# Kernel optimization log

Hardware: AMD Instinct MI355X
Metric: run time of the kernel (lower is better)

## Reference

```python
import jax, jax.numpy as jnp
import numpy as np

N = 2000  # nodes per graph (hardcoded in the original module)


def gatv2(x, src, dst, edge_attr, Wl, Wr, We, att, b):
    """PyG GATv2Conv (concat=True, negative_slope=0.2, edge_dim) forward.
    x: [N, Fin]; src/dst: [E]; edge_attr: [E, 2]; att: [H, C]. Returns [N, H*C]."""
    n = x.shape[0]
    H, C = att.shape
    xl = (x @ Wl).reshape(n, H, C)            # messages from source nodes
    xr = (x @ Wr).reshape(n, H, C)            # target-node term
    ee = (edge_attr @ We).reshape(-1, H, C)   # edge feature term
    m = jax.nn.leaky_relu(xl[src] + xr[dst] + ee, 0.2)
    logits = jnp.einsum('ehc,hc->eh', m, att)           # [E, H]
    lmax = jax.ops.segment_max(logits, dst, num_segments=n)
    p = jnp.exp(logits - lmax[dst])
    denom = jax.ops.segment_sum(p, dst, num_segments=n)
    alpha = p / (denom[dst] + 1e-16)                    # scatter-softmax over in-edges
    out = jax.ops.segment_sum(alpha[:, :, None] * xl[src], dst, num_segments=n)
    return out.reshape(n, H * C) + b


def setup_inputs() -> dict:
    key = jax.random.key(0)
    ks = jax.random.split(key, 32)
    B, T, F, E = 4, 10, 8, 16000
    s = 0.05
    d = {
        'x': jax.random.normal(ks[0], (B, T, N, F), jnp.float32),
        'edge_index': jax.random.randint(ks[1], (2, E), 0, N, jnp.int32),
        'edge_attr': jax.random.normal(ks[2], (E, 2), jnp.float32),
        'w_l0': s * jax.random.normal(ks[3], (8, 128)),
        'w_r0': s * jax.random.normal(ks[4], (8, 128)),
        'w_e0': s * jax.random.normal(ks[5], (2, 128)),
        'att0': s * jax.random.normal(ks[6], (4, 32)),
        'b0': s * jax.random.normal(ks[7], (128,)),
        'w_l1': s * jax.random.normal(ks[8], (128, 128)),
        'w_r1': s * jax.random.normal(ks[9], (128, 128)),
        'w_e1': s * jax.random.normal(ks[10], (2, 128)),
        'att1': s * jax.random.normal(ks[11], (4, 32)),
        'b1': s * jax.random.normal(ks[12], (128,)),
        'w_l2': s * jax.random.normal(ks[13], (128, 32)),
        'w_r2': s * jax.random.normal(ks[14], (128, 32)),
        'w_e2': s * jax.random.normal(ks[15], (2, 32)),
        'att2': s * jax.random.normal(ks[16], (4, 8)),
        'b2': s * jax.random.normal(ks[17], (32,)),
        'w_ih': s * jax.random.normal(ks[18], (1024, 64000)),
        'w_hh': s * jax.random.normal(ks[19], (1024, 256)),
        'b_ih': s * jax.random.normal(ks[20], (1024,)),
        'b_hh': s * jax.random.normal(ks[21], (1024,)),
        'fc1_w': s * jax.random.normal(ks[22], (256, 512)),
        'fc1_b': s * jax.random.normal(ks[23], (512,)),
        'fc2_w': s * jax.random.normal(ks[24], (512, 1)),
        'fc2_b': s * jax.random.normal(ks[25], (1,)),
    }
    return d


def reference(x, edge_index, edge_attr, w_l0, w_r0, w_e0, att0, b0,
              w_l1, w_r1, w_e1, att1, b1, w_l2, w_r2, w_e2, att2, b2,
              w_ih, w_hh, b_ih, b_hh, fc1_w, fc1_b, fc2_w, fc2_b):
    B, T = x.shape[0], x.shape[1]
    # PyG GATv2Conv add_self_loops=True with fill_value='mean' for edge_attr
    loop = jnp.arange(N, dtype=edge_index.dtype)
    src = jnp.concatenate([edge_index[0], loop])
    dst = jnp.concatenate([edge_index[1], loop])
    ea = jnp.concatenate([edge_attr, jnp.broadcast_to(edge_attr.mean(0), (N, 2))], axis=0)

    def gat_stack(xt):  # [N, F] -> [N*32] flattened embedding
        h = jax.nn.relu(gatv2(xt, src, dst, ea, w_l0, w_r0, w_e0, att0, b0))
        h = jax.nn.relu(gatv2(h, src, dst, ea, w_l1, w_r1, w_e1, att1, b1))
        h = jax.nn.relu(gatv2(h, src, dst, ea, w_l2, w_r2, w_e2, att2, b2))
        return h.reshape(-1)

    emb = jax.vmap(jax.vmap(gat_stack))(x)  # [B, T, 64000]

    # single-layer LSTM (torch gate order: i, f, g, o)
    Hh = w_hh.shape[1]
    def step(carry, xt):
        h, c = carry
        g = xt @ w_ih.T + h @ w_hh.T + (b_ih + b_hh)
        i, f, gg, o = jnp.split(g, 4, axis=-1)
        c = jax.nn.sigmoid(f) * c + jax.nn.sigmoid(i) * jnp.tanh(gg)
        h = jax.nn.sigmoid(o) * jnp.tanh(c)
        return (h, c), h
    h0 = jnp.zeros((B, Hh), emb.dtype)
    (_, _), hs = jax.lax.scan(step, (h0, h0), jnp.swapaxes(emb, 0, 1))  # hs: [T, B, Hh]

    last = jax.nn.relu(hs[-1])                       # relu(lstm_out)[:, -1, :]
    hid = jax.nn.relu(last @ fc1_w + fc1_b)          # (dropout=0 -> identity)
    return hid @ fc2_w + fc2_b                       # [B, 1]
```

## Files before the change

kernel.cpp:

```cpp
#include <hip/hip_runtime.h>
#include <hip/hip_bf16.h>
#include <math.h>

typedef __hip_bfloat16 bf16;
typedef __attribute__((ext_vector_type(8))) short short8;
typedef __attribute__((ext_vector_type(4))) float f32x4;

#define NNODES 2000
#define NEDGE_IN 16000
#define NEDGE 18000
#define NGRAPH 40

__device__ __forceinline__ float bf2f(bf16 v){ return __bfloat162float(v); }
__device__ __forceinline__ bf16 f2bf(float v){ return __float2bfloat16(v); }
__device__ __forceinline__ short bfbits(float v){ bf16 t = __float2bfloat16(v); return *reinterpret_cast<short*>(&t); }

__global__ __launch_bounds__(256) void k_setup(const float* __restrict__ ea, float* __restrict__ mean_ea,
                        const float* __restrict__ whh, unsigned* __restrict__ whhT2,
                        const float* __restrict__ w1a, const float* __restrict__ w1b,
                        const float* __restrict__ w2a, const float* __restrict__ w2b,
                        bf16* __restrict__ b1a, bf16* __restrict__ b1b,
                        bf16* __restrict__ b2a, bf16* __restrict__ b2b,
                        int* __restrict__ cnt, int* __restrict__ cursor, float* __restrict__ gates){
  int bb = blockIdx.x, tid = threadIdx.x;
  if (bb == 0){
    __shared__ float s0l[256], s1l[256];
    float s0=0.f, s1=0.f;
    for (int e = tid; e < NEDGE_IN; e += 256){ s0 += ea[2*e]; s1 += ea[2*e+1]; }
    s0l[tid]=s0; s1l[tid]=s1; __syncthreads();
    for (int d=128; d>=1; d>>=1){
      if (tid < d){ s0l[tid]+=s0l[tid+d]; s1l[tid]+=s1l[tid+d]; }
      __syncthreads();
    }
    if (tid==0){ mean_ea[0]=s0l[0]/(float)NEDGE_IN; mean_ea[1]=s1l[0]/(float)NEDGE_IN; }
  } else if (bb < 513){
    int idx = (bb-1)*256 + tid;
    int j = idx >> 7, kp = idx & 127;
    unsigned ulo = (unsigned)(unsigned short)bfbits(whh[j*256 + 2*kp]);
    unsigned uhi = (unsigned)(unsigned short)bfbits(whh[j*256 + 2*kp + 1]);
    whhT2[kp*1024 + j] = (uhi<<16) | ulo;
  } else if (bb < 673){
    int idx = (bb-513)*256 + tid;
    const float* src; bf16* dst; int n, local;
    if (idx < 16384){ src=w1a; dst=b1a; n=128; local=idx; }
    else if (idx < 32768){ src=w1b; dst=b1b; n=128; local=idx-16384; }
    else if (idx < 36864){ src=w2a; dst=b2a; n=32; local=idx-32768; }
    else { src=w2b; dst=b2b; n=32; local=idx-36864; }
    int k = local / n, c = local % n;
    dst[c*128 + k] = f2bf(src[local]);
  } else {
    int idx = (bb-673)*256 + tid;
    if (idx < 2000) cnt[idx] = 0;
    else if (idx < 4000) cursor[idx-2000] = 0;
    else if (idx < 44960) gates[idx-4000] = 0.f;
  }
}

__global__ void k_count(const int* __restrict__ ei, int* __restrict__ cnt){
  int e = blockIdx.x*256 + threadIdx.x;
  if (e >= NEDGE) return;
  int d = (e < NEDGE_IN) ? ei[NEDGE_IN + e] : (e - NEDGE_IN);
  atomicAdd(&cnt[d], 1);
}

__global__ void k_scan(const int* __restrict__ cnt, int* __restrict__ off){
  __shared__ int s[2048];
  int lane = threadIdx.x;
  for (int i = lane; i < 2048; i += 64) s[i] = (i < NNODES) ? cnt[i] : 0;
  __syncthreads();
  int base = lane*32, run = 0;
  for (int j=0;j<32;j++){ int t = s[base+j]; s[base+j] = run; run += t; }
  int x = run;
  for (int d=1; d<64; d<<=1){ int y = __shfl_up(x, d); if (lane >= d) x += y; }
  int chunkOff = x - run;
  for (int j=0;j<32;j++){ int idx = base+j; if (idx <= NNODES) off[idx] = chunkOff + s[idx]; }
}

__global__ void k_scatter(const int* __restrict__ ei, const int* __restrict__ off,
                          int* __restrict__ cursor, const float* __restrict__ ea,
                          const float* __restrict__ mean_ea,
                          int* __restrict__ csr_src, float2* __restrict__ eaP){
  int e = blockIdx.x*256 + threadIdx.x;
  if (e >= NEDGE) return;
  int d, sn; float2 a;
  if (e < NEDGE_IN){ sn = ei[e]; d = ei[NEDGE_IN+e]; a = ((const float2*)ea)[e]; }
  else { sn = e-NEDGE_IN; d = sn; a.x = mean_ea[0]; a.y = mean_ea[1]; }
  int p = off[d] + atomicAdd(&cursor[d], 1);
  csr_src[p] = sn;
  eaP[p] = a;
}

__global__ __launch_bounds__(256) void k_gemm0(const float* __restrict__ X, const float* __restrict__ Wa,
                                               const float* __restrict__ Wb,
                                               bf16* __restrict__ Ya, bf16* __restrict__ Yb){
  __shared__ float Ws[2*8*128];
  for (int i = threadIdx.x; i < 8*128; i += 256){ Ws[i] = Wa[i]; Ws[1024+i] = Wb[i]; }
  __syncthreads();
  int j  = threadIdx.x % 128;
  int rg = threadIdx.x / 128;
  size_t m0 = (size_t)blockIdx.x*8 + (size_t)rg*4;
  const float* x0 = X + m0*8;
  float a0=0.f,a1=0.f,a2=0.f,a3=0.f, b0=0.f,b1=0.f,b2=0.f,b3=0.f;
  #pragma unroll
  for (int k=0;k<8;k++){
    float wa = Ws[k*128 + j], wb = Ws[1024 + k*128 + j];
    float x_0 = x0[k], x_1 = x0[8+k], x_2 = x0[16+k], x_3 = x0[24+k];
    a0 += x_0*wa; a1 += x_1*wa; a2 += x_2*wa; a3 += x_3*wa;
    b0 += x_0*wb; b1 += x_1*wb; b2 += x_2*wb; b3 += x_3*wb;
  }
  bf16* ya = Ya + m0*128 + j;
  bf16* yb = Yb + m0*128 + j;
  ya[0]=f2bf(a0); ya[128]=f2bf(a1); ya[256]=f2bf(a2); ya[384]=f2bf(a3);
  yb[0]=f2bf(b0); yb[128]=f2bf(b1); yb[256]=f2bf(b2); yb[384]=f2bf(b3);
}

template<int N>
__global__ __launch_bounds__(256) void k_gemm_mf2(const bf16* __restrict__ A, const bf16* __restrict__ BTa,
                                                  const bf16* __restrict__ BTb,
                                                  bf16* __restrict__ Ya, bf16* __restrict__ Yb){
  const int NT = N/16;
  int lane = threadIdx.x & 63, wv = threadIdx.x >> 6;
  size_t m0 = (size_t)blockIdx.x*128 + (size_t)wv*32;
  int r = lane & 15, kg = lane >> 4;
  const f32x4 zero = {0.f,0.f,0.f,0.f};
  f32x4 acca[2][NT], accb[2][NT];
  #pragma unroll
  for (int s=0;s<2;s++)
    #pragma unroll
    for (int t=0;t<NT;t++){ acca[s][t] = zero; accb[s][t] = zero; }
  #pragma unroll
  for (int c=0;c<4;c++){
    short8 a0 = *(const short8*)(A + (m0 + r)*128 + c*32 + kg*8);
    short8 a1 = *(const short8*)(A + (m0 + 16 + r)*128 + c*32 + kg*8);
    #pragma unroll
    for (int t=0;t<NT;t++){
      short8 ba = *(const short8*)(BTa + (size_t)(t*16 + r)*128 + c*32 + kg*8);
      short8 bb = *(const short8*)(BTb + (size_t)(t*16 + r)*128 + c*32 + kg*8);
      acca[0][t] = __builtin_amdgcn_mfma_f32_16x16x32_bf16(a0, ba, acca[0][t], 0,0,0);
      acca[1][t] = __builtin_amdgcn_mfma_f32_16x16x32_bf16(a1, ba, acca[1][t], 0,0,0);
      accb[0][t] = __builtin_amdgcn_mfma_f32_16x16x32_bf16(a0, bb, accb[0][t], 0,0,0);
      accb[1][t] = __builtin_amdgcn_mfma_f32_16x16x32_bf16(a1, bb, accb[1][t], 0,0,0);
    }
  }
  #pragma unroll
  for (int s=0;s<2;s++)
    #pragma unroll
    for (int t=0;t<NT;t++){
      size_t row = m0 + s*16 + kg*4;
      int col = t*16 + r;
      #pragma unroll
      for (int i=0;i<4;i++){
        Ya[(row+i)*N + col] = f2bf(acca[s][t][i]);
        Yb[(row+i)*N + col] = f2bf(accb[s][t][i]);
      }
    }
}

template<int H, int C>
__global__ __launch_bounds__(256) void k_edge(const bf16* __restrict__ XL, const bf16* __restrict__ XR,
                                              const float2* __restrict__ eaP, const int* __restrict__ off,
                                              const int* __restrict__ csr_src, const float* __restrict__ att,
                                              const float* __restrict__ We, const float* __restrict__ bias,
                                              bf16* __restrict__ Hout){
  const int HC = H*C;
  const int LPN = HC/2;
  const int NPW = 64/LPN;
  const int NPB = 4*NPW;
  int tid = threadIdx.x;
  int lane = tid & 63, wv = tid >> 6;
  int ln = lane % LPN;
  int n  = blockIdx.x*NPB + wv*NPW + lane/LPN;
  int g  = blockIdx.y;
  int c0 = 2*ln;
  size_t gbase = (size_t)g*NNODES*HC;
  const unsigned* XLu = (const unsigned*)(XL + gbase);
  unsigned xru = ((const unsigned*)(XR + gbase))[n*LPN + ln];
  float xr0 = __uint_as_float(xru<<16);
  float xr1 = __uint_as_float(xru & 0xffff0000u);
  float av0 = att[c0], av1 = att[c0+1];
  float w00 = We[c0], w01 = We[c0+1];
  float w10 = We[HC+c0], w11 = We[HC+c0+1];
  float srun = 0.f, acc0 = 0.f, acc1 = 0.f;
  int p0 = off[n], p1 = off[n+1];
  int p = p0;
  for (; p+2 <= p1; p += 2){
    int uA = csr_src[p], uB = csr_src[p+1];
    float2 eA = eaP[p], eB = eaP[p+1];
    unsigned xlA = XLu[uA*LPN + ln];
    unsigned xlB = XLu[uB*LPN + ln];
    float xa0 = __uint_as_float(xlA<<16), xa1 = __uint_as_float(xlA & 0xffff0000u);
    float xb0 = __uint_as_float(xlB<<16), xb1 = __uint_as_float(xlB & 0xffff0000u);
    float sa0 = xa0 + fmaf(eA.x,w00, fmaf(eA.y,w10, xr0));
    float sa1 = xa1 + fmaf(eA.x,w01, fmaf(eA.y,w11, xr1));
    float sb0 = xb0 + fmaf(eB.x,w00, fmaf(eB.y,w10, xr0));
    float sb1 = xb1 + fmaf(eB.x,w01, fmaf(eB.y,w11, xr1));
    float ma0 = sa0>0.f?sa0:0.2f*sa0, ma1 = sa1>0.f?sa1:0.2f*sa1;
    float mb0 = sb0>0.f?sb0:0.2f*sb0, mb1 = sb1>0.f?sb1:0.2f*sb1;
    float cA = fmaf(ma0,av0, ma1*av1);
    float cB = fmaf(mb0,av0, mb1*av1);
    #pragma unroll
    for (int d=C/4; d>=1; d>>=1){ cA += __shfl_xor(cA, d); cB += __shfl_xor(cB, d); }
    float peA = __expf(cA), peB = __expf(cB);
    srun += peA + peB;
    acc0 = fmaf(peA, xa0, fmaf(peB, xb0, acc0));
    acc1 = fmaf(peA, xa1, fmaf(peB, xb1, acc1));
  }
  if (p < p1){
    int uA = csr_src[p];
    float2 eA = eaP[p];
    unsigned xlA = XLu[uA*LPN + ln];
    float xa0 = __uint_as_float(xlA<<16), xa1 = __uint_as_float(xlA & 0xffff0000u);
    float sa0 = xa0 + fmaf(eA.x,w00, fmaf(eA.y,w10, xr0));
    float sa1 = xa1 + fmaf(eA.x,w01, fmaf(eA.y,w11, xr1));
    float ma0 = sa0>0.f?sa0:0.2f*sa0, ma1 = sa1>0.f?sa1:0.2f*sa1;
    float cA = fmaf(ma0,av0, ma1*av1);
    #pragma unroll
    for (int d=C/4; d>=1; d>>=1) cA += __shfl_xor(cA, d);
    float peA = __expf(cA);
    srun += peA;
    acc0 = fmaf(peA, xa0, acc0);
    acc1 = fmaf(peA, xa1, acc1);
  }
  float inv = 1.f/(srun + 1e-16f);
  float o0 = fmaf(acc0, inv, bias[c0]);
  float o1 = fmaf(acc1, inv, bias[c0+1]);
  o0 = o0>0.f?o0:0.f; o1 = o1>0.f?o1:0.f;
  unsigned r0 = (unsigned)(unsigned short)bfbits(o0);
  unsigned r1 = (unsigned)(unsigned short)bfbits(o1);
  ((unsigned*)(Hout + gbase))[n*LPN + ln] = (r1<<16) | r0;
}

#define GATES_KS 40
__global__ __launch_bounds__(256) void k_gates_mf(const bf16* __restrict__ emb, const float* __restrict__ wih,
                                                  float* __restrict__ gates){
  const int nk = 2000/GATES_KS;
  int lane = threadIdx.x & 63, wv = threadIdx.x >> 6;
  int r = lane & 15, kg = lane >> 4;
  int j0 = (blockIdx.x*4 + wv)*16;
  int k0 = blockIdx.y*nk*32;
  const f32x4 zero = {0.f,0.f,0.f,0.f};
  f32x4 acc0 = zero, acc1 = zero, acc2 = zero;
  const float* wrow = wih + (size_t)(j0 + r)*64000;
  const bf16*  e0p  = emb + (size_t)r*64000;
  const bf16*  e1p  = emb + (size_t)(16+r)*64000;
  const bf16*  e2p  = emb + (size_t)(32+r)*64000;
  #pragma unroll 2
  for (int s=0; s<nk; ++s){
    int k = k0 + s*32 + kg*8;
    float4 wa = *(const float4*)(wrow + k);
    float4 wb = *(const float4*)(wrow + k + 4);
    short8 bfr;
    bfr[0]=bfbits(wa.x); bfr[1]=bfbits(wa.y); bfr[2]=bfbits(wa.z); bfr[3]=bfbits(wa.w);
    bfr[4]=bfbits(wb.x); bfr[5]=bfbits(wb.y); bfr[6]=bfbits(wb.z); bfr[7]=bfbits(wb.w);
    short8 a0 = *(const short8*)(e0p + k);
    short8 a1 = *(const short8*)(e1p + k);
    short8 a2 = *(const short8*)(e2p + k);
    acc0 = __builtin_amdgcn_mfma_f32_16x16x32_bf16(a0, bfr, acc0, 0,0,0);
    acc1 = __builtin_amdgcn_mfma_f32_16x16x32_bf16(a1, bfr, acc1, 0,0,0);
    acc2 = __builtin_amdgcn_mfma_f32_16x16x32_bf16(a2, bfr, acc2, 0,0,0);
  }
  int col = j0 + r;
  #pragma unroll
  for (int i=0;i<4;i++){
    int row = kg*4 + i;
    atomicAdd(&gates[(size_t)row*1024 + col], acc0[i]);
    atomicAdd(&gates[(size_t)(row+16)*1024 + col], acc1[i]);
    if (row + 32 < 40) atomicAdd(&gates[(size_t)(row+32)*1024 + col], acc2[i]);
  }
}

__global__ __launch_bounds__(1024) void k_lstm10(const float* __restrict__ gates, const unsigned* __restrict__ whhT2,
                                                 const float* __restrict__ bih, const float* __restrict__ bhh,
                                                 float* __restrict__ hst){
  __shared__ float hs[256];
  __shared__ float g[1024];
  int b = blockIdx.x, j = threadIdx.x;
  float c_reg = 0.f;
  if (j < 256) hs[j] = 0.f;
  float bias = bih[j] + bhh[j];
  __syncthreads();
  for (int t=0;t<10;t++){
    float acc = gates[(size_t)(b*10+t)*1024 + j] + bias;
    #pragma unroll 16
    for (int kp=0;kp<128;kp++){
      unsigned u = whhT2[kp*1024 + j];
      float2 h2 = *(const float2*)&hs[2*kp];
      acc = fmaf(__uint_as_float(u<<16), h2.x, acc);
      acc = fmaf(__uint_as_float(u & 0xffff0000u), h2.y, acc);
    }
    g[j] = acc;
    __syncthreads();
    if (j < 256){
      float i_ = g[j], f_ = g[j+256], gg = g[j+512], o_ = g[j+768];
      float si = 1.f/(1.f+__expf(-i_));
      float sf = 1.f/(1.f+__expf(-f_));
      float so = 1.f/(1.f+__expf(-o_));
      c_reg = sf*c_reg + si*tanhf(gg);
      float hn = so*tanhf(c_reg);
      hs[j] = hn;
      if (t==9) hst[b*256+j] = hn;
    }
    __syncthreads();
  }
}

__global__ __launch_bounds__(512) void k_head(const float* __restrict__ hst, const float* __restrict__ fc1w,
                                              const float* __restrict__ fc1b, const float* __restrict__ fc2w,
                                              const float* __restrict__ fc2b, float* __restrict__ out){
  __shared__ float r[512];
  int b = blockIdx.x, j = threadIdx.x;
  float acc = fc1b[j];
  for (int k=0;k<256;k++){
    float l = hst[b*256+k]; l = l>0.f?l:0.f;
    acc += l * fc1w[k*512 + j];
  }
  float hid = acc>0.f?acc:0.f;
  r[j] = hid * fc2w[j];
  __syncthreads();
  for (int d=256; d>=1; d>>=1){ if (j<d) r[j]+=r[j+d]; __syncthreads(); }
  if (j==0) out[b] = r[0] + fc2b[0];
}

extern "C" void kernel_launch(void* const* d_in, const int* in_sizes, int n_in,
                              void* d_out, int out_size, void* d_ws, size_t ws_size,
                              hipStream_t stream){
  const float* x    = (const float*)d_in[0];
  const int*   ei   = (const int*)  d_in[1];
  const float* ea   = (const float*)d_in[2];
  const float* wl0  = (const float*)d_in[3];
  const float* wr0  = (const float*)d_in[4];
  const float* we0  = (const float*)d_in[5];
  const float* att0 = (const float*)d_in[6];
  const float* b0   = (const float*)d_in[7];
  const float* wl1  = (const float*)d_in[8];
  const float* wr1  = (const float*)d_in[9];
  const float* we1  = (const float*)d_in[10];
  const float* att1 = (const float*)d_in[11];
  const float* b1   = (const float*)d_in[12];
  const float* wl2  = (const float*)d_in[13];
  const float* wr2  = (const float*)d_in[14];
  const float* we2  = (const float*)d_in[15];
  const float* att2 = (const float*)d_in[16];
  const float* b2   = (const float*)d_in[17];
  const float* wih  = (const float*)d_in[18];
  const float* whh  = (const float*)d_in[19];
  const float* bih  = (const float*)d_in[20];
  const float* bhh  = (const float*)d_in[21];
  const float* fc1w = (const float*)d_in[22];
  const float* fc1b = (const float*)d_in[23];
  const float* fc2w = (const float*)d_in[24];
  const float* fc2b = (const float*)d_in[25];
  float* out = (float*)d_out;

  char* base = (char*)d_ws; size_t cur = 0;
  auto alloc = [&](size_t bytes)->void*{
    cur = (cur + 255) & ~(size_t)255; void* p = base + cur; cur += bytes; return p;
  };
  float* mean_ea = (float*)alloc(8);
  int*   cnt     = (int*)  alloc((size_t)NNODES*4);
  int*   off     = (int*)  alloc((size_t)(NNODES+1)*4);
  int*   cursor  = (int*)  alloc((size_t)NNODES*4);
  int*   csr_src = (int*)  alloc((size_t)NEDGE*4);
  float2* eaP    = (float2*)alloc((size_t)NEDGE*8);
  bf16*  XL      = (bf16*) alloc((size_t)80000*128*2);
  bf16*  XR      = (bf16*) alloc((size_t)80000*128*2);
  bf16*  HBUF    = (bf16*) alloc((size_t)80000*128*2);
  float* gates   = (float*)alloc((size_t)40*1024*4);
  float* hst     = (float*)alloc(4*256*4);
  unsigned* whhT2= (unsigned*)alloc((size_t)128*1024*4);
  bf16*  bt1a    = (bf16*) alloc((size_t)128*128*2);
  bf16*  bt1b    = (bf16*) alloc((size_t)128*128*2);
  bf16*  bt2a    = (bf16*) alloc((size_t)32*128*2);
  bf16*  bt2b    = (bf16*) alloc((size_t)32*128*2);

  k_setup <<<849,256,0,stream>>>(ea, mean_ea, whh, whhT2, wl1, wr1, wl2, wr2,
                                 bt1a, bt1b, bt2a, bt2b, cnt, cursor, gates);
  k_count   <<<(NEDGE+255)/256,256,0,stream>>>(ei, cnt);
  k_scan    <<<1,64,0,stream>>>(cnt, off);
  k_scatter <<<(NEDGE+255)/256,256,0,stream>>>(ei, off, cursor, ea, mean_ea, csr_src, eaP);

  k_gemm0   <<<10000,256,0,stream>>>(x, wl0, wr0, XL, XR);
  k_edge<4,32> <<<dim3(500,40),256,0,stream>>>(XL,XR,eaP,off,csr_src,att0,we0,b0,HBUF);

  k_gemm_mf2<128> <<<625,256,0,stream>>>(HBUF, bt1a, bt1b, XL, XR);
  k_edge<4,32> <<<dim3(500,40),256,0,stream>>>(XL,XR,eaP,off,csr_src,att1,we1,b1,HBUF);

  k_gemm_mf2<32> <<<625,256,0,stream>>>(HBUF, bt2a, bt2b, XL, XR);
  k_edge<4,8> <<<dim3(125,40),256,0,stream>>>(XL,XR,eaP,off,csr_src,att2,we2,b2,HBUF);

  k_gates_mf<<<dim3(16,GATES_KS),256,0,stream>>>(HBUF, wih, gates);

  k_lstm10<<<4,1024,0,stream>>>(gates, whhT2, bih, bhh, hst);

  k_head<<<4,512,0,stream>>>(hst, fc1w, fc1b, fc2w, fc2b, out);
}
```

Before: 430.4 us.

## Fuse CSR build into one block, software-pipeline edge loop, widen LSTM weight loads

Merges the mean, count, scan and scatter kernels into a single 1024-thread block that works in shared memory, which cuts launches and global atomics. The edge kernel loop becomes single-edge with a one-ahead prefetch of the next source row, replacing the two-edge unroll. The LSTM recurrence now reads W_hh through 8-byte uint2 loads with a relaid-out transposed matrix. The CSR build on one block serialises work onto a single CU, and the edge loop change may lower instruction-level parallelism.

```diff
diff --git a/kernel.cpp b/kernel.cpp
--- a/kernel.cpp
+++ b/kernel.cpp
@@ -14,33 +14,24 @@
 __device__ __forceinline__ float bf2f(bf16 v){ return __bfloat162float(v); }
 __device__ __forceinline__ bf16 f2bf(float v){ return __float2bfloat16(v); }
 __device__ __forceinline__ short bfbits(float v){ bf16 t = __float2bfloat16(v); return *reinterpret_cast<short*>(&t); }
-
-__global__ __launch_bounds__(256) void k_setup(const float* __restrict__ ea, float* __restrict__ mean_ea,
-                        const float* __restrict__ whh, unsigned* __restrict__ whhT2,
+__device__ __forceinline__ float blo(unsigned u){ return __uint_as_float(u<<16); }
+__device__ __forceinline__ float bhi(unsigned u){ return __uint_as_float(u & 0xffff0000u); }
+
+__global__ __launch_bounds__(256) void k_setup(const float* __restrict__ whh, unsigned* __restrict__ whhT2,
                         const float* __restrict__ w1a, const float* __restrict__ w1b,
                         const float* __restrict__ w2a, const float* __restrict__ w2b,
                         bf16* __restrict__ b1a, bf16* __restrict__ b1b,
                         bf16* __restrict__ b2a, bf16* __restrict__ b2b,
-                        int* __restrict__ cnt, int* __restrict__ cursor, float* __restrict__ gates){
+                        float* __restrict__ gates){
   int bb = blockIdx.x, tid = threadIdx.x;
-  if (bb == 0){
-    __shared__ float s0l[256], s1l[256];
-    float s0=0.f, s1=0.f;
-    for (int e = tid; e < NEDGE_IN; e += 256){ s0 += ea[2*e]; s1 += ea[2*e+1]; }
-    s0l[tid]=s0; s1l[tid]=s1; __syncthreads();
-    for (int d=128; d>=1; d>>=1){
-      if (tid < d){ s0l[tid]+=s0l[tid+d]; s1l[tid]+=s1l[tid+d]; }
-      __syncthreads();
-    }
-    if (tid==0){ mean_ea[0]=s0l[0]/(float)NEDGE_IN; mean_ea[1]=s1l[0]/(float)NEDGE_IN; }
-  } else if (bb < 513){
-    int idx = (bb-1)*256 + tid;
+  if (bb < 512){
+    int idx = bb*256 + tid;
     int j = idx >> 7, kp = idx & 127;
     unsigned ulo = (unsigned)(unsigned short)bfbits(whh[j*256 + 2*kp]);
     unsigned uhi = (unsigned)(unsigned short)bfbits(whh[j*256 + 2*kp + 1]);
-    whhT2[kp*1024 + j] = (uhi<<16) | ulo;
-  } else if (bb < 673){
-    int idx = (bb-513)*256 + tid;
+    whhT2[(kp>>1)*2048 + 2*j + (kp&1)] = (uhi<<16) | ulo;
+  } else if (bb < 672){
+    int idx = (bb-512)*256 + tid;
     const float* src; bf16* dst; int n, local;
     if (idx < 16384){ src=w1a; dst=b1a; n=128; local=idx; }
     else if (idx < 32768){ src=w1b; dst=b1b; n=128; local=idx-16384; }
@@ -49,45 +40,56 @@
     int k = local / n, c = local % n;
     dst[c*128 + k] = f2bf(src[local]);
   } else {
-    int idx = (bb-673)*256 + tid;
-    if (idx < 2000) cnt[idx] = 0;
-    else if (idx < 4000) cursor[idx-2000] = 0;
-    else if (idx < 44960) gates[idx-4000] = 0.f;
-  }
-}
-
-__global__ void k_count(const int* __restrict__ ei, int* __restrict__ cnt){
-  int e = blockIdx.x*256 + threadIdx.x;
-  if (e >= NEDGE) return;
-  int d = (e < NEDGE_IN) ? ei[NEDGE_IN + e] : (e - NEDGE_IN);
-  atomicAdd(&cnt[d], 1);
-}
-
-__global__ void k_scan(const int* __restrict__ cnt, int* __restrict__ off){
-  __shared__ int s[2048];
-  int lane = threadIdx.x;
-  for (int i = lane; i < 2048; i += 64) s[i] = (i < NNODES) ? cnt[i] : 0;
-  __syncthreads();
-  int base = lane*32, run = 0;
-  for (int j=0;j<32;j++){ int t = s[base+j]; s[base+j] = run; run += t; }
-  int x = run;
-  for (int d=1; d<64; d<<=1){ int y = __shfl_up(x, d); if (lane >= d) x += y; }
-  int chunkOff = x - run;
-  for (int j=0;j<32;j++){ int idx = base+j; if (idx <= NNODES) off[idx] = chunkOff + s[idx]; }
-}
-
-__global__ void k_scatter(const int* __restrict__ ei, const int* __restrict__ off,
-                          int* __restrict__ cursor, const float* __restrict__ ea,
-                          const float* __restrict__ mean_ea,
-                          int* __restrict__ csr_src, float2* __restrict__ eaP){
-  int e = blockIdx.x*256 + threadIdx.x;
-  if (e >= NEDGE) return;
-  int d, sn; float2 a;
-  if (e < NEDGE_IN){ sn = ei[e]; d = ei[NEDGE_IN+e]; a = ((const float2*)ea)[e]; }
-  else { sn = e-NEDGE_IN; d = sn; a.x = mean_ea[0]; a.y = mean_ea[1]; }
-  int p = off[d] + atomicAdd(&cursor[d], 1);
-  csr_src[p] = sn;
-  eaP[p] = a;
+    int idx = (bb-672)*256 + tid;
+    if (idx < 40960) gates[idx] = 0.f;
+  }
+}
+
+__global__ __launch_bounds__(1024) void k_graph(const int* __restrict__ ei, const float* __restrict__ ea,
+                                                int* __restrict__ off_g, int* __restrict__ csr_src,
+                                                float2* __restrict__ eaP){
+  __shared__ float red[1024];
+  __shared__ float mean0, mean1;
+  __shared__ int cnt[2048];
+  __shared__ int cur[2000];
+  __shared__ int off[2001];
+  int tid = threadIdx.x;
+  float s0=0.f, s1=0.f;
+  for (int e=tid; e<NEDGE_IN; e+=1024){ float2 a = ((const float2*)ea)[e]; s0+=a.x; s1+=a.y; }
+  red[tid]=s0; __syncthreads();
+  for (int d=512; d>=1; d>>=1){ if(tid<d) red[tid]+=red[tid+d]; __syncthreads(); }
+  if (tid==0) mean0 = red[0]/(float)NEDGE_IN;
+  __syncthreads();
+  red[tid]=s1; __syncthreads();
+  for (int d=512; d>=1; d>>=1){ if(tid<d) red[tid]+=red[tid+d]; __syncthreads(); }
+  if (tid==0) mean1 = red[0]/(float)NEDGE_IN;
+  for (int i=tid; i<2048; i+=1024) cnt[i]=0;
+  for (int i=tid; i<2000; i+=1024) cur[i]=0;
+  __syncthreads();
+  for (int e=tid; e<NEDGE; e+=1024){
+    int d = (e < NEDGE_IN) ? ei[NEDGE_IN+e] : (e-NEDGE_IN);
+    atomicAdd(&cnt[d], 1);
+  }
+  __syncthreads();
+  if (tid < 64){
+    int lane = tid;
+    int base = lane*32, run = 0;
+    for (int j=0;j<32;j++){ int t = cnt[base+j]; cnt[base+j] = run; run += t; }
+    int x = run;
+    for (int d=1; d<64; d<<=1){ int y = __shfl_up(x, d); if (lane >= d) x += y; }
+    int chunkOff = x - run;
+    for (int j=0;j<32;j++){ int idx = base+j; if (idx <= NNODES) off[idx] = chunkOff + cnt[idx]; }
+  }
+  __syncthreads();
+  for (int e=tid; e<NEDGE; e+=1024){
+    int d, sn; float2 a;
+    if (e < NEDGE_IN){ sn = ei[e]; d = ei[NEDGE_IN+e]; a = ((const float2*)ea)[e]; }
+    else { sn = e-NEDGE_IN; d = sn; a.x = mean0; a.y = mean1; }
+    int p = off[d] + atomicAdd(&cur[d], 1);
+    csr_src[p] = sn;
+    eaP[p] = a;
+  }
+  for (int i=tid; i<=NNODES; i+=1024) off_g[i] = off[i];
 }
 
 __global__ __launch_bounds__(256) void k_gemm0(const float* __restrict__ X, const float* __restrict__ Wa,
@@ -175,51 +177,32 @@
   size_t gbase = (size_t)g*NNODES*HC;
   const unsigned* XLu = (const unsigned*)(XL + gbase);
   unsigned xru = ((const unsigned*)(XR + gbase))[n*LPN + ln];
-  float xr0 = __uint_as_float(xru<<16);
-  float xr1 = __uint_as_float(xru & 0xffff0000u);
+  float xr0 = blo(xru), xr1 = bhi(xru);
   float av0 = att[c0], av1 = att[c0+1];
   float w00 = We[c0], w01 = We[c0+1];
   float w10 = We[HC+c0], w11 = We[HC+c0+1];
   float srun = 0.f, acc0 = 0.f, acc1 = 0.f;
-  int p0 = off[n], p1 = off[n+1];
-  int p = p0;
-  for (; p+2 <= p1; p += 2){
-    int uA = csr_src[p], uB = csr_src[p+1];
-    float2 eA = eaP[p], eB = eaP[p+1];
-    unsigned xlA = XLu[uA*LPN + ln];
-    unsigned xlB = XLu[uB*LPN + ln];
-    float xa0 = __uint_as_float(xlA<<16), xa1 = __uint_as_float(xlA & 0xffff0000u);
-    float xb0 = __uint_as_float(xlB<<16), xb1 = __uint_as_float(xlB & 0xffff0000u);
-    float sa0 = xa0 + fmaf(eA.x,w00, fmaf(eA.y,w10, xr0));
-    float sa1 = xa1 + fmaf(eA.x,w01, fmaf(eA.y,w11, xr1));
-    float sb0 = xb0 + fmaf(eB.x,w00, fmaf(eB.y,w10, xr0));
-    float sb1 = xb1 + fmaf(eB.x,w01, fmaf(eB.y,w11, xr1));
-    float ma0 = sa0>0.f?sa0:0.2f*sa0, ma1 = sa1>0.f?sa1:0.2f*sa1;
-    float mb0 = sb0>0.f?sb0:0.2f*sb0, mb1 = sb1>0.f?sb1:0.2f*sb1;
-    float cA = fmaf(ma0,av0, ma1*av1);
-    float cB = fmaf(mb0,av0, mb1*av1);
+  int p0v = off[n], p1v = off[n+1];
+  int u = csr_src[p0v];
+  float2 e2 = eaP[p0v];
+  unsigned xl = XLu[u*LPN + ln];
+  for (int p = p0v; p < p1v; ++p){
+    int pn = (p+1 < p1v) ? p+1 : p;
+    int un = csr_src[pn];
+    float2 en = eaP[pn];
+    unsigned xln = XLu[un*LPN + ln];
+    float x0 = blo(xl), x1 = bhi(xl);
+    float s0 = x0 + fmaf(e2.x,w00, fmaf(e2.y,w10, xr0));
+    float s1 = x1 + fmaf(e2.x,w01, fmaf(e2.y,w11, xr1));
+    float m0 = s0>0.f?s0:0.2f*s0, m1 = s1>0.f?s1:0.2f*s1;
+    float c = fmaf(m0,av0, m1*av1);
     #pragma unroll
-    for (int d=C/4; d>=1; d>>=1){ cA += __shfl_xor(cA, d); cB += __shfl_xor(cB, d); }
-    float peA = __expf(cA), peB = __expf(cB);
-    srun += peA + peB;
-    acc0 = fmaf(peA, xa0, fmaf(peB, xb0, acc0));
-    acc1 = fmaf(peA, xa1, fmaf(peB, xb1, acc1));
-  }
-  if (p < p1){
-    int uA = csr_src[p];
-    float2 eA = eaP[p];
-    unsigned xlA = XLu[uA*LPN + ln];
-    float xa0 = __uint_as_float(xlA<<16), xa1 = __uint_as_float(xlA & 0xffff0000u);
-    float sa0 = xa0 + fmaf(eA.x,w00, fmaf(eA.y,w10, xr0));
-    float sa1 = xa1 + fmaf(eA.x,w01, fmaf(eA.y,w11, xr1));
-    float ma0 = sa0>0.f?sa0:0.2f*sa0, ma1 = sa1>0.f?sa1:0.2f*sa1;
-    float cA = fmaf(ma0,av0, ma1*av1);
-    #pragma unroll
-    for (int d=C/4; d>=1; d>>=1) cA += __shfl_xor(cA, d);
-    float peA = __expf(cA);
-    srun += peA;
-    acc0 = fmaf(peA, xa0, acc0);
-    acc1 = fmaf(peA, xa1, acc1);
+    for (int d=C/4; d>=1; d>>=1) c += __shfl_xor(c, d);
+    float pe = __expf(c);
+    srun += pe;
+    acc0 = fmaf(pe, x0, acc0);
+    acc1 = fmaf(pe, x1, acc1);
+    u = un; e2 = en; xl = xln;
   }
   float inv = 1.f/(srun + 1e-16f);
   float o0 = fmaf(acc0, inv, bias[c0]);
@@ -278,15 +261,18 @@
   float c_reg = 0.f;
   if (j < 256) hs[j] = 0.f;
   float bias = bih[j] + bhh[j];
+  const uint2* w4 = (const uint2*)whhT2;
   __syncthreads();
   for (int t=0;t<10;t++){
     float acc = gates[(size_t)(b*10+t)*1024 + j] + bias;
-    #pragma unroll 16
-    for (int kp=0;kp<128;kp++){
-      unsigned u = whhT2[kp*1024 + j];
-      float2 h2 = *(const float2*)&hs[2*kp];
-      acc = fmaf(__uint_as_float(u<<16), h2.x, acc);
-      acc = fmaf(__uint_as_float(u & 0xffff0000u), h2.y, acc);
+    #pragma unroll 8
+    for (int kp2=0;kp2<64;kp2++){
+      uint2 u = w4[kp2*1024 + j];
+      float4 h4 = *(const float4*)&hs[4*kp2];
+      acc = fmaf(blo(u.x), h4.x, acc);
+      acc = fmaf(bhi(u.x), h4.y, acc);
+      acc = fmaf(blo(u.y), h4.z, acc);
+      acc = fmaf(bhi(u.y), h4.w, acc);
     }
     g[j] = acc;
     __syncthreads();
@@ -356,10 +342,7 @@
   auto alloc = [&](size_t bytes)->void*{
     cur = (cur + 255) & ~(size_t)255; void* p = base + cur; cur += bytes; return p;
   };
-  float* mean_ea = (float*)alloc(8);
-  int*   cnt     = (int*)  alloc((size_t)NNODES*4);
   int*   off     = (int*)  alloc((size_t)(NNODES+1)*4);
-  int*   cursor  = (int*)  alloc((size_t)NNODES*4);
   int*   csr_src = (int*)  alloc((size_t)NEDGE*4);
   float2* eaP    = (float2*)alloc((size_t)NEDGE*8);
   bf16*  XL      = (bf16*) alloc((size_t)80000*128*2);
@@ -373,11 +356,9 @@
   bf16*  bt2a    = (bf16*) alloc((size_t)32*128*2);
   bf16*  bt2b    = (bf16*) alloc((size_t)32*128*2);
 
-  k_setup <<<849,256,0,stream>>>(ea, mean_ea, whh, whhT2, wl1, wr1, wl2, wr2,
-                                 bt1a, bt1b, bt2a, bt2b, cnt, cursor, gates);
-  k_count   <<<(NEDGE+255)/256,256,0,stream>>>(ei, cnt);
-  k_scan    <<<1,64,0,stream>>>(cnt, off);
-  k_scatter <<<(NEDGE+255)/256,256,0,stream>>>(ei, off, cursor, ea, mean_ea, csr_src, eaP);
+  k_setup <<<832,256,0,stream>>>(whh, whhT2, wl1, wr1, wl2, wr2,
+                                 bt1a, bt1b, bt2a, bt2b, gates);
+  k_graph <<<1,1024,0,stream>>>(ei, ea, off, csr_src, eaP);
 
   k_gemm0   <<<10000,256,0,stream>>>(x, wl0, wr0, XL, XR);
   k_edge<4,32> <<<dim3(500,40),256,0,stream>>>(XL,XR,eaP,off,csr_src,att0,we0,b0,HBUF);
```

Measured after the change: 555.5 us. +29.1%, slower.
